# Optimization experiments

Measured on AMD Instinct MI355X. Metric: run time of the kernel, lower is better.

The kernel has to match this reference:

```python
import jax, jax.numpy as jnp
import numpy as np

N, E, G = 50000, 640000, 1024
D, RD, H = 128, 200, 512
NUM_ATOM_FEATS, ATOM_VOCAB = 9, 64
NUM_BOND_FEATS, BOND_VOCAB = 3, 16


def setup_inputs() -> dict:
    key = jax.random.key(0)
    ks = jax.random.split(key, 24)
    inp = {
        "x_feat": jax.random.randint(ks[0], (N, NUM_ATOM_FEATS), 0, ATOM_VOCAB),
        "edge_index": jax.random.randint(ks[1], (2, E), 0, N),
        "edge_attr_feat": jax.random.randint(ks[2], (E, NUM_BOND_FEATS), 0, BOND_VOCAB),
        "batch": jnp.sort(jax.random.randint(ks[3], (N,), 0, G)),
        "rdkit_feats": jax.random.normal(ks[4], (G, RD), dtype=jnp.float32),
        # learned params
        "atom_emb": jax.random.normal(ks[5], (NUM_ATOM_FEATS, ATOM_VOCAB, D), dtype=jnp.float32) * 0.02,
        "bond_emb": jax.random.normal(ks[6], (NUM_BOND_FEATS, BOND_VOCAB, D), dtype=jnp.float32) * 0.02,
        "conv1_w1": jax.random.normal(ks[7], (D, D), dtype=jnp.float32) / np.sqrt(D),
        "conv1_b1": jnp.zeros((D,), jnp.float32),
        "conv1_w2": jax.random.normal(ks[8], (D, D), dtype=jnp.float32) / np.sqrt(D),
        "conv1_b2": jnp.zeros((D,), jnp.float32),
        "conv2_w1": jax.random.normal(ks[9], (D, D), dtype=jnp.float32) / np.sqrt(D),
        "conv2_b1": jnp.zeros((D,), jnp.float32),
        "conv2_w2": jax.random.normal(ks[10], (D, D), dtype=jnp.float32) / np.sqrt(D),
        "conv2_b2": jnp.zeros((D,), jnp.float32),
        "mlp_w1": jax.random.normal(ks[11], (D + RD, H), dtype=jnp.float32) / np.sqrt(D + RD),
        "mlp_b1": jnp.zeros((H,), jnp.float32),
        "mlp_w2": jax.random.normal(ks[12], (H, H // 2), dtype=jnp.float32) / np.sqrt(H),
        "mlp_b2": jnp.zeros((H // 2,), jnp.float32),
        "mlp_w3": jax.random.normal(ks[13], (H // 2, 1), dtype=jnp.float32) / np.sqrt(H // 2),
        "mlp_b3": jnp.zeros((1,), jnp.float32),
    }
    return inp


def _gine_conv(x, edge_index, edge_attr, w1, b1, w2, b2, eps=0.0):
    # PyG GINEConv: out = nn((1+eps)*x + sum_{j in N(i)} relu(x_j + e_ji))
    src, dst = edge_index[0], edge_index[1]
    msg = jax.nn.relu(x[src] + edge_attr)               # [E, D]
    agg = jax.ops.segment_sum(msg, dst, num_segments=x.shape[0])  # [N, D]
    h = (1.0 + eps) * x + agg
    h = jax.nn.relu(h @ w1 + b1)
    return h @ w2 + b2


def reference(x_feat, edge_index, edge_attr_feat, batch, rdkit_feats,
              atom_emb, bond_emb,
              conv1_w1, conv1_b1, conv1_w2, conv1_b2,
              conv2_w1, conv2_b1, conv2_w2, conv2_b2,
              mlp_w1, mlp_b1, mlp_w2, mlp_b2, mlp_w3, mlp_b3):
    # AtomEncoder / BondEncoder: sum of per-feature categorical embeddings
    x = atom_emb[jnp.arange(NUM_ATOM_FEATS)[None, :], x_feat].sum(axis=1)          # [N, D]
    edge_attr = bond_emb[jnp.arange(NUM_BOND_FEATS)[None, :], edge_attr_feat].sum(axis=1)  # [E, D]

    x = _gine_conv(x, edge_index, edge_attr, conv1_w1, conv1_b1, conv1_w2, conv1_b2)
    x = _gine_conv(x, edge_index, edge_attr, conv2_w1, conv2_b1, conv2_w2, conv2_b2)

    # global mean pool over graphs
    sums = jax.ops.segment_sum(x, batch, num_segments=G)                # [G, D]
    counts = jax.ops.segment_sum(jnp.ones((x.shape[0],), x.dtype), batch, num_segments=G)
    pooled = sums / jnp.maximum(counts, 1.0)[:, None]

    h = jnp.concatenate([pooled, rdkit_feats], axis=1)                  # [G, D+RD]
    h = jax.nn.relu(h @ mlp_w1 + mlp_b1)   # dropout is identity in eval mode
    h = jax.nn.relu(h @ mlp_w2 + mlp_b2)
    return h @ mlp_w3 + mlp_b3                                          # [G, 1]
```

## Files before the change

### kernel.cpp

```cpp
#include <hip/hip_runtime.h>

#define N_NODES 50000
#define N_EDGES 640000
#define N_GRAPH 1024
#define D 128
#define RD 200
#define CAP 64

typedef __attribute__((ext_vector_type(4))) float f32x4;
typedef __attribute__((ext_vector_type(8))) float f32x8;
typedef __attribute__((ext_vector_type(4))) _Float16 half4;
typedef __attribute__((ext_vector_type(8))) _Float16 half8;

__global__ void k_prep(const float* __restrict__ w0, const float* __restrict__ w1,
                       const float* __restrict__ w2, const float* __restrict__ w3,
                       const float* __restrict__ mw1, const float* __restrict__ mw2,
                       const float* __restrict__ emb,
                       _Float16* __restrict__ cWf,
                       _Float16* __restrict__ W1f,
                       _Float16* __restrict__ W2f,
                       _Float16* __restrict__ embh,
                       int* __restrict__ deg) {
  int t = blockIdx.x * 256 + threadIdx.x;
  if (t < N_NODES) deg[t] = 0;
  if (t < 8192) {
    int mat = t >> 11, r = t & 2047;
    int frag = r >> 6, lane = r & 63;
    int n0 = frag >> 2, kk = frag & 3;
    int n = n0 * 16 + (lane & 15);
    int kb = (lane >> 4) * 8 + kk * 32;
    const float* W = (mat == 0) ? w0 : (mat == 1) ? w1 : (mat == 2) ? w2 : w3;
    half8 o;
#pragma unroll
    for (int j = 0; j < 8; ++j) o[j] = (_Float16)W[(kb + j) * D + n];
    *(half8*)&cWf[((size_t)mat * 2048 + r) * 8] = o;
  } else if (t < 8192 + 22528) {
    int u = t - 8192;
    int frag = u >> 6, lane = u & 63;
    int n0 = frag / 11, kk = frag % 11;
    int n = n0 * 16 + (lane & 15);
    int kb = (lane >> 4) * 8 + kk * 32;
    half8 o;
#pragma unroll
    for (int j = 0; j < 8; ++j) {
      int k = kb + j;
      o[j] = (k < 328) ? (_Float16)mw1[k * 512 + n] : (_Float16)0.f;
    }
    *(half8*)&W1f[(size_t)u * 8] = o;
  } else if (t < 8192 + 22528 + 16384) {
    int u = t - 8192 - 22528;
    int frag = u >> 6, lane = u & 63;
    int n0 = frag >> 4, kk = frag & 15;
    int n = n0 * 16 + (lane & 15);
    int kb = (lane >> 4) * 8 + kk * 32;
    half8 o;
#pragma unroll
    for (int j = 0; j < 8; ++j) o[j] = (_Float16)mw2[(kb + j) * 256 + n];
    *(half8*)&W2f[(size_t)u * 8] = o;
  } else if (t < 8192 + 22528 + 16384 + 9216) {
    int u = t - 8192 - 22528 - 16384;
    float4 v0 = *(const float4*)&emb[(size_t)u * 8];
    float4 v1 = *(const float4*)&emb[(size_t)u * 8 + 4];
    half8 o;
    o[0] = (_Float16)v0.x; o[1] = (_Float16)v0.y; o[2] = (_Float16)v0.z; o[3] = (_Float16)v0.w;
    o[4] = (_Float16)v1.x; o[5] = (_Float16)v1.y; o[6] = (_Float16)v1.z; o[7] = (_Float16)v1.w;
    *(half8*)&embh[(size_t)u * 8] = o;
  }
}

__global__ void k_atom_count(const int* __restrict__ xf, const _Float16* __restrict__ embh,
                             _Float16* __restrict__ x16,
                             const int* __restrict__ ei, const int* __restrict__ bondf,
                             const int* __restrict__ batch,
                             int* __restrict__ deg, int2* __restrict__ drep,
                             int* __restrict__ gstart) {
  if (blockIdx.x < 3125) {
    int t = blockIdx.x * 256 + threadIdx.x;
    int node = t >> 4, c = (t & 15) << 3;
    if ((t & 15) == 0) {
      int b = batch[node];
      int prev = (node == 0) ? -1 : batch[node - 1];
      for (int g = prev + 1; g <= b; ++g) gstart[g] = node;
      if (node == N_NODES - 1)
        for (int g = b + 1; g <= N_GRAPH; ++g) gstart[g] = N_NODES;
    }
    int v[9];
#pragma unroll
    for (int f = 0; f < 9; ++f) v[f] = xf[node * 9 + f];
    f32x8 a = (f32x8)(0.f);
#pragma unroll
    for (int f = 0; f < 9; ++f) {
      half8 e8 = *(const half8*)&embh[(size_t)(f * 64 + v[f]) * D + c];
      a += __builtin_convertvector(e8, f32x8);
    }
    half8 o;
#pragma unroll
    for (int tt = 0; tt < 8; ++tt) o[tt] = (_Float16)a[tt];
    *(half8*)&x16[(size_t)node * D + c] = o;
  } else {
    int e = (blockIdx.x - 3125) * 256 + threadIdx.x;
    if (e < N_EDGES) {
      int d = ei[N_EDGES + e];
      int rank = atomicAdd(&deg[d], 1);
      int s = ei[e];
      int f0 = bondf[e * 3], f1 = bondf[e * 3 + 1], f2 = bondf[e * 3 + 2];
      drep[e] = make_int2(d | (rank << 16), s | (f0 << 16) | (f1 << 20) | (f2 << 24));
    }
  }
}

__global__ void k_fill(const int2* __restrict__ drep, int* __restrict__ csr1) {
  int e = blockIdx.x * 256 + threadIdx.x;
  if (e >= N_EDGES) return;
  int2 v = drep[e];
  int d = v.x & 0xFFFF;
  int rank = ((unsigned)v.x) >> 16;
  if (rank < CAP) csr1[(d << 6) | rank] = v.y;
}

__global__ __launch_bounds__(256) void k_agg(
    const _Float16* __restrict__ X, const int* __restrict__ deg,
    const int* __restrict__ csr1, const float* __restrict__ bemb,
    _Float16* __restrict__ out) {
  __shared__ half8 sB[48 * 16];
  for (int t = threadIdx.x; t < 768; t += blockDim.x) {
    float4 v0 = *(const float4*)&bemb[t * 8];
    float4 v1 = *(const float4*)&bemb[t * 8 + 4];
    half8 h;
    h[0] = (_Float16)v0.x; h[1] = (_Float16)v0.y; h[2] = (_Float16)v0.z; h[3] = (_Float16)v0.w;
    h[4] = (_Float16)v1.x; h[5] = (_Float16)v1.y; h[6] = (_Float16)v1.z; h[7] = (_Float16)v1.w;
    sB[t] = h;
  }
  __syncthreads();
  int lane = threadIdx.x & 63;
  int quad = lane >> 4, l15 = lane & 15, c8 = l15 * 8;
  int wid = blockIdx.x * 4 + (threadIdx.x >> 6);
  int nw = gridDim.x * 4;
  if (wid >= N_NODES) return;
  int pdeg = deg[wid];
  int pcreg = csr1[(wid << 6) + lane];
  for (int i = wid; i < N_NODES; i += nw) {
    int degn = pdeg;
    int creg = pcreg;
    int i2 = (i + nw < N_NODES) ? i + nw : i;
    pdeg = deg[i2];
    pcreg = csr1[(i2 << 6) + lane];
    int dq = degn > CAP ? CAP : degn;
    f32x8 ac0 = (f32x8)(0.f), ac1 = (f32x8)(0.f);
    for (int jb = 0; jb < dq; jb += 8) {
      unsigned e0v = (unsigned)__shfl(creg, jb + quad);
      unsigned e1v = (unsigned)__shfl(creg, jb + 4 + quad);
      if (jb + quad < dq) {
        half8 x0 = *(const half8*)&X[(size_t)(e0v & 0xFFFF) * D + c8];
        unsigned p0 = e0v >> 16;
        half8 m0h = (x0 + sB[(p0 & 15) * 16 + l15]) +
                    (sB[256 + ((p0 >> 4) & 15) * 16 + l15] + sB[512 + (p0 >> 8) * 16 + l15]);
        f32x8 g0 = __builtin_convertvector(m0h, f32x8);
#pragma unroll
        for (int tt = 0; tt < 8; ++tt) ac0[tt] += fmaxf(g0[tt], 0.f);
      }
      if (jb + 4 + quad < dq) {
        half8 x1 = *(const half8*)&X[(size_t)(e1v & 0xFFFF) * D + c8];
        unsigned p1 = e1v >> 16;
        half8 m1h = (x1 + sB[(p1 & 15) * 16 + l15]) +
                    (sB[256 + ((p1 >> 4) & 15) * 16 + l15] + sB[512 + (p1 >> 8) * 16 + l15]);
        f32x8 g1 = __builtin_convertvector(m1h, f32x8);
#pragma unroll
        for (int tt = 0; tt < 8; ++tt) ac1[tt] += fmaxf(g1[tt], 0.f);
      }
    }
    f32x8 acc = ac0 + ac1;
#pragma unroll
    for (int tt = 0; tt < 8; ++tt) {
      acc[tt] += __shfl_xor(acc[tt], 16);
      acc[tt] += __shfl_xor(acc[tt], 32);
    }
    if (quad == 0) {
      half8 sr = *(const half8*)&X[(size_t)i * D + c8];
      f32x8 o = __builtin_convertvector(sr, f32x8) + acc;
      half8 oh;
#pragma unroll
      for (int tt = 0; tt < 8; ++tt) oh[tt] = (_Float16)o[tt];
      *(half8*)&out[(size_t)i * D + c8] = oh;
    }
  }
}

__global__ __launch_bounds__(256) void k_conv(
    const _Float16* __restrict__ A,
    const _Float16* __restrict__ W1f, const float* __restrict__ b1,
    const _Float16* __restrict__ W2f, const float* __restrict__ b2,
    _Float16* __restrict__ O16) {
  __shared__ _Float16 sW[2048 * 8];
  __shared__ _Float16 sI[128 * 136];
  int tid = threadIdx.x, w = tid >> 6, lane = tid & 63;
  int m0 = blockIdx.x * 128;
  int col16 = lane & 15, q = lane >> 4;
  for (int t = tid; t < 2048; t += 256)
    *(float4*)&sW[t * 8] = *(const float4*)&W1f[(size_t)t * 8];
  half8 afr[2][4];
#pragma unroll
  for (int f = 0; f < 2; ++f) {
    int row = m0 + w * 32 + f * 16 + col16;
    if (row >= N_NODES) row = N_NODES - 1;
    const _Float16* Ar = A + (size_t)row * D + q * 8;
#pragma unroll
    for (int kk = 0; kk < 4; ++kk) afr[f][kk] = *(const half8*)(Ar + kk * 32);
  }
  __syncthreads();
#pragma unroll
  for (int n0 = 0; n0 < 8; ++n0) {
    f32x4 a0 = {0.f, 0.f, 0.f, 0.f}, a1 = {0.f, 0.f, 0.f, 0.f};
#pragma unroll
    for (int kk = 0; kk < 4; ++kk) {
      half8 b = *(const half8*)&sW[((n0 * 4 + kk) * 64 + lane) * 8];
      a0 = __builtin_amdgcn_mfma_f32_16x16x32_f16(afr[0][kk], b, a0, 0, 0, 0);
      a1 = __builtin_amdgcn_mfma_f32_16x16x32_f16(afr[1][kk], b, a1, 0, 0, 0);
    }
    float bb = b1[n0 * 16 + col16];
#pragma unroll
    for (int r = 0; r < 4; ++r) {
      sI[(w * 32 + q * 4 + r) * 136 + n0 * 16 + col16] = (_Float16)fmaxf(a0[r] + bb, 0.f);
      sI[(w * 32 + 16 + q * 4 + r) * 136 + n0 * 16 + col16] = (_Float16)fmaxf(a1[r] + bb, 0.f);
    }
  }
  __syncthreads();
  for (int t = tid; t < 2048; t += 256)
    *(float4*)&sW[t * 8] = *(const float4*)&W2f[(size_t)t * 8];
  half8 a2[2][4];
#pragma unroll
  for (int f = 0; f < 2; ++f) {
    const _Float16* tr = &sI[(w * 32 + f * 16 + col16) * 136 + q * 8];
#pragma unroll
    for (int kk = 0; kk < 4; ++kk) a2[f][kk] = *(const half8*)(tr + kk * 32);
  }
  __syncthreads();
#pragma unroll
  for (int n0 = 0; n0 < 8; ++n0) {
    f32x4 a0 = {0.f, 0.f, 0.f, 0.f}, a1 = {0.f, 0.f, 0.f, 0.f};
#pragma unroll
    for (int kk = 0; kk < 4; ++kk) {
      half8 b = *(const half8*)&sW[((n0 * 4 + kk) * 64 + lane) * 8];
      a0 = __builtin_amdgcn_mfma_f32_16x16x32_f16(a2[0][kk], b, a0, 0, 0, 0);
      a1 = __builtin_amdgcn_mfma_f32_16x16x32_f16(a2[1][kk], b, a1, 0, 0, 0);
    }
    int col = n0 * 16 + col16;
    float bb = b2[col];
#pragma unroll
    for (int r = 0; r < 4; ++r) {
      int r0 = m0 + w * 32 + q * 4 + r;
      int r1 = r0 + 16;
      if (r0 < N_NODES) O16[(size_t)r0 * D + col] = (_Float16)(a0[r] + bb);
      if (r1 < N_NODES) O16[(size_t)r1 * D + col] = (_Float16)(a1[r] + bb);
    }
  }
}

__global__ __launch_bounds__(256) void k_pool(
    const _Float16* __restrict__ x, const int* __restrict__ gstart,
    const float* __restrict__ rdkit, _Float16* __restrict__ hcat,
    const float* __restrict__ B3, float* __restrict__ out) {
  int g = blockIdx.x * 4 + (threadIdx.x >> 6);
  if (g >= N_GRAPH) return;
  int lane = threadIdx.x & 63;
  int half_ = lane >> 5;
  int c4 = (lane & 31) * 4;
  int lo = gstart[g];
  int hi = gstart[g + 1];
  f32x4 a = {0.f, 0.f, 0.f, 0.f};
  for (int i = lo + half_; i < hi; i += 2) {
    half4 v = *(const half4*)&x[(size_t)i * D + c4];
    a += __builtin_convertvector(v, f32x4);
  }
#pragma unroll
  for (int t = 0; t < 4; ++t) a[t] += __shfl_xor(a[t], 32);
  float inv = 1.f / fmaxf((float)(hi - lo), 1.f);
  if (half_ == 0) {
    half4 o;
    o.x = (_Float16)(a[0] * inv); o.y = (_Float16)(a[1] * inv);
    o.z = (_Float16)(a[2] * inv); o.w = (_Float16)(a[3] * inv);
    *(half4*)&hcat[(size_t)g * 352 + c4] = o;
  }
  for (int r = lane; r < RD; r += 64)
    hcat[(size_t)g * 352 + D + r] = (_Float16)rdkit[(size_t)g * RD + r];
  if (lane < 24) hcat[(size_t)g * 352 + 328 + lane] = (_Float16)0.f;
  if (lane == 0) out[g] = B3[0];
}

__global__ __launch_bounds__(512) void k_mlp(
    const _Float16* __restrict__ A, const _Float16* __restrict__ W1f,
    const float* __restrict__ B1, const _Float16* __restrict__ W2f,
    const float* __restrict__ B2, const float* __restrict__ W3,
    float* __restrict__ out) {
  __shared__ _Float16 sH1[16 * 520];
  int tid = threadIdx.x, w = tid >> 6, lane = tid & 63;
  int mt = blockIdx.x;
  int col16 = lane & 15, q = lane >> 4;
  {
    half8 afr[11];
    const _Float16* Ar = A + (size_t)(mt * 16 + col16) * 352 + q * 8;
#pragma unroll
    for (int kk = 0; kk < 11; ++kk) afr[kk] = *(const half8*)(Ar + kk * 32);
#pragma unroll
    for (int ng = 0; ng < 4; ++ng) {
      int n0 = w * 4 + ng;
      f32x4 acc = {0.f, 0.f, 0.f, 0.f};
#pragma unroll
      for (int kk = 0; kk < 11; ++kk) {
        half8 b = *(const half8*)&W1f[(size_t)((n0 * 11 + kk) * 64 + lane) * 8];
        acc = __builtin_amdgcn_mfma_f32_16x16x32_f16(afr[kk], b, acc, 0, 0, 0);
      }
      int col = n0 * 16 + col16;
      float bb = B1[col];
#pragma unroll
      for (int r = 0; r < 4; ++r)
        sH1[(q * 4 + r) * 520 + col] = (_Float16)fmaxf(acc[r] + bb, 0.f);
    }
  }
  __syncthreads();
  {
    half8 a2[16];
    const _Float16* Ar = &sH1[col16 * 520 + q * 8];
#pragma unroll
    for (int kk = 0; kk < 16; ++kk) a2[kk] = *(const half8*)(Ar + kk * 32);
    float p[4] = {0.f, 0.f, 0.f, 0.f};
#pragma unroll
    for (int ng = 0; ng < 2; ++ng) {
      int n0 = w * 2 + ng;
      f32x4 acc = {0.f, 0.f, 0.f, 0.f};
#pragma unroll
      for (int kk = 0; kk < 16; ++kk) {
        half8 b = *(const half8*)&W2f[(size_t)((n0 * 16 + kk) * 64 + lane) * 8];
        acc = __builtin_amdgcn_mfma_f32_16x16x32_f16(a2[kk], b, acc, 0, 0, 0);
      }
      int col = n0 * 16 + col16;
      float bb = B2[col], w3 = W3[col];
#pragma unroll
      for (int r = 0; r < 4; ++r) p[r] += fmaxf(acc[r] + bb, 0.f) * w3;
    }
#pragma unroll
    for (int r = 0; r < 4; ++r) {
      p[r] += __shfl_xor(p[r], 1);
      p[r] += __shfl_xor(p[r], 2);
      p[r] += __shfl_xor(p[r], 4);
      p[r] += __shfl_xor(p[r], 8);
    }
    if (col16 == 0) {
#pragma unroll
      for (int r = 0; r < 4; ++r)
        atomicAdd(&out[mt * 16 + q * 4 + r], p[r]);
    }
  }
}

extern "C" void kernel_launch(void* const* d_in, const int* in_sizes, int n_in,
                              void* d_out, int out_size, void* d_ws, size_t ws_size,
                              hipStream_t stream) {
  const int* x_feat = (const int*)d_in[0];
  const int* ei = (const int*)d_in[1];
  const int* bondf = (const int*)d_in[2];
  const int* batch = (const int*)d_in[3];
  const float* rdkit = (const float*)d_in[4];
  const float* atom_emb = (const float*)d_in[5];
  const float* bond_emb = (const float*)d_in[6];
  const float* c1w1 = (const float*)d_in[7];
  const float* c1b1 = (const float*)d_in[8];
  const float* c1w2 = (const float*)d_in[9];
  const float* c1b2 = (const float*)d_in[10];
  const float* c2w1 = (const float*)d_in[11];
  const float* c2b1 = (const float*)d_in[12];
  const float* c2w2 = (const float*)d_in[13];
  const float* c2b2 = (const float*)d_in[14];
  const float* mw1 = (const float*)d_in[15];
  const float* mb1 = (const float*)d_in[16];
  const float* mw2 = (const float*)d_in[17];
  const float* mb2 = (const float*)d_in[18];
  const float* mw3 = (const float*)d_in[19];
  const float* mb3 = (const float*)d_in[20];
  float* out = (float*)d_out;

  char* ws = (char*)d_ws;
  size_t off = 0;
  auto alloc = [&](size_t bytes) {
    void* p = ws + off;
    off += (bytes + 255) & ~(size_t)255;
    return p;
  };
  _Float16* x16a = (_Float16*)alloc((size_t)N_NODES * D * 2);
  _Float16* x16b = (_Float16*)alloc((size_t)N_NODES * D * 2);
  _Float16* h16 = (_Float16*)alloc((size_t)N_NODES * D * 2);
  _Float16* x2_16 = (_Float16*)alloc((size_t)N_NODES * D * 2);
  int* deg = (int*)alloc((size_t)N_NODES * 4);
  int* csr1 = (int*)alloc((size_t)N_NODES * CAP * 4);
  int2* drep = (int2*)alloc((size_t)N_EDGES * 8);
  int* gstart = (int*)alloc((size_t)(N_GRAPH + 1) * 4);
  _Float16* hcat16 = (_Float16*)alloc((size_t)N_GRAPH * 352 * 2);
  _Float16* cWf = (_Float16*)alloc((size_t)4 * 2048 * 8 * 2);
  _Float16* W1f = (_Float16*)alloc((size_t)352 * 64 * 8 * 2);
  _Float16* W2f = (_Float16*)alloc((size_t)256 * 64 * 8 * 2);
  _Float16* embh = (_Float16*)alloc((size_t)9 * 64 * D * 2);

  k_prep<<<256, 256, 0, stream>>>(c1w1, c1w2, c2w1, c2w2, mw1, mw2, atom_emb,
                                  cWf, W1f, W2f, embh, deg);
  k_atom_count<<<3125 + 2500, 256, 0, stream>>>(x_feat, embh, x16a,
                                                ei, bondf, batch,
                                                deg, drep, gstart);
  k_fill<<<(N_EDGES + 255) / 256, 256, 0, stream>>>(drep, csr1);

  int ctiles = (N_NODES + 127) / 128;
  k_agg<<<2048, 256, 0, stream>>>(x16a, deg, csr1, bond_emb, h16);
  k_conv<<<ctiles, 256, 0, stream>>>(h16, cWf + 0 * 16384, c1b1,
                                     cWf + 1 * 16384, c1b2, x16b);
  k_agg<<<2048, 256, 0, stream>>>(x16b, deg, csr1, bond_emb, h16);
  k_conv<<<ctiles, 256, 0, stream>>>(h16, cWf + 2 * 16384, c2b1,
                                     cWf + 3 * 16384, c2b2, x2_16);

  k_pool<<<N_GRAPH / 4, 256, 0, stream>>>(x2_16, gstart, rdkit, hcat16, mb3, out);
  k_mlp<<<N_GRAPH / 16, 512, 0, stream>>>(hcat16, W1f, mb1, W2f, mb2, mw3, out);

  (void)in_sizes; (void)n_in; (void)out_size; (void)ws_size;
}
```

Measured before the change: 266.1 us.

## Fuse prep, atom encoding, and CSR fill; merge pooling into MLP head

Folds weight-fragment prep and degree zeroing into the atom-encoder kernel, which now reads the fp32 atom embeddings directly instead of a converted fp16 copy. The edge counting and CSR scatter become a single kernel, removing the intermediate drep buffer and one launch. The mean pool is merged into the MLP kernel through shared memory, eliminating the hcat round trip and another launch. In exchange, pooling runs on only 64 blocks, which lowers parallelism for that phase.

```diff
diff --git a/kernel.cpp b/kernel.cpp
--- a/kernel.cpp
+++ b/kernel.cpp
@@ -12,68 +12,16 @@
 typedef __attribute__((ext_vector_type(4))) _Float16 half4;
 typedef __attribute__((ext_vector_type(8))) _Float16 half8;
 
-__global__ void k_prep(const float* __restrict__ w0, const float* __restrict__ w1,
-                       const float* __restrict__ w2, const float* __restrict__ w3,
-                       const float* __restrict__ mw1, const float* __restrict__ mw2,
-                       const float* __restrict__ emb,
-                       _Float16* __restrict__ cWf,
-                       _Float16* __restrict__ W1f,
-                       _Float16* __restrict__ W2f,
-                       _Float16* __restrict__ embh,
-                       int* __restrict__ deg) {
-  int t = blockIdx.x * 256 + threadIdx.x;
-  if (t < N_NODES) deg[t] = 0;
-  if (t < 8192) {
-    int mat = t >> 11, r = t & 2047;
-    int frag = r >> 6, lane = r & 63;
-    int n0 = frag >> 2, kk = frag & 3;
-    int n = n0 * 16 + (lane & 15);
-    int kb = (lane >> 4) * 8 + kk * 32;
-    const float* W = (mat == 0) ? w0 : (mat == 1) ? w1 : (mat == 2) ? w2 : w3;
-    half8 o;
-#pragma unroll
-    for (int j = 0; j < 8; ++j) o[j] = (_Float16)W[(kb + j) * D + n];
-    *(half8*)&cWf[((size_t)mat * 2048 + r) * 8] = o;
-  } else if (t < 8192 + 22528) {
-    int u = t - 8192;
-    int frag = u >> 6, lane = u & 63;
-    int n0 = frag / 11, kk = frag % 11;
-    int n = n0 * 16 + (lane & 15);
-    int kb = (lane >> 4) * 8 + kk * 32;
-    half8 o;
-#pragma unroll
-    for (int j = 0; j < 8; ++j) {
-      int k = kb + j;
-      o[j] = (k < 328) ? (_Float16)mw1[k * 512 + n] : (_Float16)0.f;
-    }
-    *(half8*)&W1f[(size_t)u * 8] = o;
-  } else if (t < 8192 + 22528 + 16384) {
-    int u = t - 8192 - 22528;
-    int frag = u >> 6, lane = u & 63;
-    int n0 = frag >> 4, kk = frag & 15;
-    int n = n0 * 16 + (lane & 15);
-    int kb = (lane >> 4) * 8 + kk * 32;
-    half8 o;
-#pragma unroll
-    for (int j = 0; j < 8; ++j) o[j] = (_Float16)mw2[(kb + j) * 256 + n];
-    *(half8*)&W2f[(size_t)u * 8] = o;
-  } else if (t < 8192 + 22528 + 16384 + 9216) {
-    int u = t - 8192 - 22528 - 16384;
-    float4 v0 = *(const float4*)&emb[(size_t)u * 8];
-    float4 v1 = *(const float4*)&emb[(size_t)u * 8 + 4];
-    half8 o;
-    o[0] = (_Float16)v0.x; o[1] = (_Float16)v0.y; o[2] = (_Float16)v0.z; o[3] = (_Float16)v0.w;
-    o[4] = (_Float16)v1.x; o[5] = (_Float16)v1.y; o[6] = (_Float16)v1.z; o[7] = (_Float16)v1.w;
-    *(half8*)&embh[(size_t)u * 8] = o;
-  }
-}
-
-__global__ void k_atom_count(const int* __restrict__ xf, const _Float16* __restrict__ embh,
-                             _Float16* __restrict__ x16,
-                             const int* __restrict__ ei, const int* __restrict__ bondf,
-                             const int* __restrict__ batch,
-                             int* __restrict__ deg, int2* __restrict__ drep,
-                             int* __restrict__ gstart) {
+__global__ void k_pre(const float* __restrict__ emb,
+                      const int* __restrict__ xf, const int* __restrict__ batch,
+                      const float* __restrict__ w0, const float* __restrict__ w1,
+                      const float* __restrict__ w2, const float* __restrict__ w3,
+                      const float* __restrict__ mw1, const float* __restrict__ mw2,
+                      _Float16* __restrict__ cWf,
+                      _Float16* __restrict__ W1f,
+                      _Float16* __restrict__ W2f,
+                      _Float16* __restrict__ x16, int* __restrict__ deg,
+                      int* __restrict__ gstart) {
   if (blockIdx.x < 3125) {
     int t = blockIdx.x * 256 + threadIdx.x;
     int node = t >> 4, c = (t & 15) << 3;
@@ -90,32 +38,67 @@
     f32x8 a = (f32x8)(0.f);
 #pragma unroll
     for (int f = 0; f < 9; ++f) {
-      half8 e8 = *(const half8*)&embh[(size_t)(f * 64 + v[f]) * D + c];
-      a += __builtin_convertvector(e8, f32x8);
+      const float* er = &emb[(size_t)(f * 64 + v[f]) * D + c];
+      float4 v0 = *(const float4*)er;
+      float4 v1 = *(const float4*)(er + 4);
+      a[0] += v0.x; a[1] += v0.y; a[2] += v0.z; a[3] += v0.w;
+      a[4] += v1.x; a[5] += v1.y; a[6] += v1.z; a[7] += v1.w;
     }
     half8 o;
 #pragma unroll
     for (int tt = 0; tt < 8; ++tt) o[tt] = (_Float16)a[tt];
     *(half8*)&x16[(size_t)node * D + c] = o;
   } else {
-    int e = (blockIdx.x - 3125) * 256 + threadIdx.x;
-    if (e < N_EDGES) {
-      int d = ei[N_EDGES + e];
-      int rank = atomicAdd(&deg[d], 1);
-      int s = ei[e];
-      int f0 = bondf[e * 3], f1 = bondf[e * 3 + 1], f2 = bondf[e * 3 + 2];
-      drep[e] = make_int2(d | (rank << 16), s | (f0 << 16) | (f1 << 20) | (f2 << 24));
-    }
-  }
-}
-
-__global__ void k_fill(const int2* __restrict__ drep, int* __restrict__ csr1) {
+    int u = (blockIdx.x - 3125) * 256 + threadIdx.x;
+    if (u < N_NODES) deg[u] = 0;
+    if (u < 8192) {
+      int mat = u >> 11, r = u & 2047;
+      int frag = r >> 6, lane = r & 63;
+      int n0 = frag >> 2, kk = frag & 3;
+      int n = n0 * 16 + (lane & 15);
+      int kb = (lane >> 4) * 8 + kk * 32;
+      const float* W = (mat == 0) ? w0 : (mat == 1) ? w1 : (mat == 2) ? w2 : w3;
+      half8 o;
+#pragma unroll
+      for (int j = 0; j < 8; ++j) o[j] = (_Float16)W[(kb + j) * D + n];
+      *(half8*)&cWf[((size_t)mat * 2048 + r) * 8] = o;
+    } else if (u < 8192 + 22528) {
+      int t2 = u - 8192;
+      int frag = t2 >> 6, lane = t2 & 63;
+      int n0 = frag / 11, kk = frag % 11;
+      int n = n0 * 16 + (lane & 15);
+      int kb = (lane >> 4) * 8 + kk * 32;
+      half8 o;
+#pragma unroll
+      for (int j = 0; j < 8; ++j) {
+        int k = kb + j;
+        o[j] = (k < 328) ? (_Float16)mw1[k * 512 + n] : (_Float16)0.f;
+      }
+      *(half8*)&W1f[(size_t)t2 * 8] = o;
+    } else if (u < 8192 + 22528 + 16384) {
+      int t2 = u - 8192 - 22528;
+      int frag = t2 >> 6, lane = t2 & 63;
+      int n0 = frag >> 4, kk = frag & 15;
+      int n = n0 * 16 + (lane & 15);
+      int kb = (lane >> 4) * 8 + kk * 32;
+      half8 o;
+#pragma unroll
+      for (int j = 0; j < 8; ++j) o[j] = (_Float16)mw2[(kb + j) * 256 + n];
+      *(half8*)&W2f[(size_t)t2 * 8] = o;
+    }
+  }
+}
+
+__global__ void k_fill(const int* __restrict__ ei, const int* __restrict__ bondf,
+                       int* __restrict__ deg, int* __restrict__ csr1) {
   int e = blockIdx.x * 256 + threadIdx.x;
   if (e >= N_EDGES) return;
-  int2 v = drep[e];
-  int d = v.x & 0xFFFF;
-  int rank = ((unsigned)v.x) >> 16;
-  if (rank < CAP) csr1[(d << 6) | rank] = v.y;
+  int d = ei[N_EDGES + e];
+  int rank = atomicAdd(&deg[d], 1);
+  int s = ei[e];
+  int f0 = bondf[e * 3], f1 = bondf[e * 3 + 1], f2 = bondf[e * 3 + 2];
+  if (rank < CAP)
+    csr1[(d << 6) | rank] = s | (f0 << 16) | (f1 << 20) | (f2 << 24);
 }
 
 __global__ __launch_bounds__(256) void k_agg(
@@ -256,49 +239,53 @@
   }
 }
 
-__global__ __launch_bounds__(256) void k_pool(
+__global__ __launch_bounds__(512) void k_head(
     const _Float16* __restrict__ x, const int* __restrict__ gstart,
-    const float* __restrict__ rdkit, _Float16* __restrict__ hcat,
-    const float* __restrict__ B3, float* __restrict__ out) {
-  int g = blockIdx.x * 4 + (threadIdx.x >> 6);
-  if (g >= N_GRAPH) return;
-  int lane = threadIdx.x & 63;
-  int half_ = lane >> 5;
-  int c4 = (lane & 31) * 4;
-  int lo = gstart[g];
-  int hi = gstart[g + 1];
-  f32x4 a = {0.f, 0.f, 0.f, 0.f};
-  for (int i = lo + half_; i < hi; i += 2) {
-    half4 v = *(const half4*)&x[(size_t)i * D + c4];
-    a += __builtin_convertvector(v, f32x4);
-  }
-#pragma unroll
-  for (int t = 0; t < 4; ++t) a[t] += __shfl_xor(a[t], 32);
-  float inv = 1.f / fmaxf((float)(hi - lo), 1.f);
-  if (half_ == 0) {
-    half4 o;
-    o.x = (_Float16)(a[0] * inv); o.y = (_Float16)(a[1] * inv);
-    o.z = (_Float16)(a[2] * inv); o.w = (_Float16)(a[3] * inv);
-    *(half4*)&hcat[(size_t)g * 352 + c4] = o;
-  }
-  for (int r = lane; r < RD; r += 64)
-    hcat[(size_t)g * 352 + D + r] = (_Float16)rdkit[(size_t)g * RD + r];
-  if (lane < 24) hcat[(size_t)g * 352 + 328 + lane] = (_Float16)0.f;
-  if (lane == 0) out[g] = B3[0];
-}
-
-__global__ __launch_bounds__(512) void k_mlp(
-    const _Float16* __restrict__ A, const _Float16* __restrict__ W1f,
-    const float* __restrict__ B1, const _Float16* __restrict__ W2f,
-    const float* __restrict__ B2, const float* __restrict__ W3,
+    const float* __restrict__ rdkit,
+    const _Float16* __restrict__ W1f, const float* __restrict__ B1,
+    const _Float16* __restrict__ W2f, const float* __restrict__ B2,
+    const float* __restrict__ W3, const float* __restrict__ B3,
     float* __restrict__ out) {
+  __shared__ _Float16 sH[16 * 360];
   __shared__ _Float16 sH1[16 * 520];
   int tid = threadIdx.x, w = tid >> 6, lane = tid & 63;
   int mt = blockIdx.x;
   int col16 = lane & 15, q = lane >> 4;
+
+  {
+    int half_ = lane >> 5;
+    int c4 = (lane & 31) * 4;
+#pragma unroll
+    for (int gg = 0; gg < 2; ++gg) {
+      int row = w * 2 + gg;
+      int g = mt * 16 + row;
+      int lo = gstart[g];
+      int hi = gstart[g + 1];
+      f32x4 a = {0.f, 0.f, 0.f, 0.f};
+      for (int i = lo + half_; i < hi; i += 2) {
+        half4 v = *(const half4*)&x[(size_t)i * D + c4];
+        a += __builtin_convertvector(v, f32x4);
+      }
+#pragma unroll
+      for (int t = 0; t < 4; ++t) a[t] += __shfl_xor(a[t], 32);
+      float inv = 1.f / fmaxf((float)(hi - lo), 1.f);
+      if (half_ == 0) {
+        half4 o;
+        o.x = (_Float16)(a[0] * inv); o.y = (_Float16)(a[1] * inv);
+        o.z = (_Float16)(a[2] * inv); o.w = (_Float16)(a[3] * inv);
+        *(half4*)&sH[row * 360 + c4] = o;
+      }
+      for (int r = lane; r < RD; r += 64)
+        sH[row * 360 + D + r] = (_Float16)rdkit[(size_t)g * RD + r];
+      if (lane < 24) sH[row * 360 + 328 + lane] = (_Float16)0.f;
+      if (lane == 0) out[g] = B3[0];
+    }
+  }
+  __syncthreads();
+
   {
     half8 afr[11];
-    const _Float16* Ar = A + (size_t)(mt * 16 + col16) * 352 + q * 8;
+    const _Float16* Ar = &sH[col16 * 360 + q * 8];
 #pragma unroll
     for (int kk = 0; kk < 11; ++kk) afr[kk] = *(const half8*)(Ar + kk * 32);
 #pragma unroll
@@ -318,6 +305,7 @@
     }
   }
   __syncthreads();
+
   {
     half8 a2[16];
     const _Float16* Ar = &sH1[col16 * 520 + q * 8];
@@ -392,20 +380,15 @@
   _Float16* x2_16 = (_Float16*)alloc((size_t)N_NODES * D * 2);
   int* deg = (int*)alloc((size_t)N_NODES * 4);
   int* csr1 = (int*)alloc((size_t)N_NODES * CAP * 4);
-  int2* drep = (int2*)alloc((size_t)N_EDGES * 8);
   int* gstart = (int*)alloc((size_t)(N_GRAPH + 1) * 4);
-  _Float16* hcat16 = (_Float16*)alloc((size_t)N_GRAPH * 352 * 2);
   _Float16* cWf = (_Float16*)alloc((size_t)4 * 2048 * 8 * 2);
   _Float16* W1f = (_Float16*)alloc((size_t)352 * 64 * 8 * 2);
   _Float16* W2f = (_Float16*)alloc((size_t)256 * 64 * 8 * 2);
-  _Float16* embh = (_Float16*)alloc((size_t)9 * 64 * D * 2);
-
-  k_prep<<<256, 256, 0, stream>>>(c1w1, c1w2, c2w1, c2w2, mw1, mw2, atom_emb,
-                                  cWf, W1f, W2f, embh, deg);
-  k_atom_count<<<3125 + 2500, 256, 0, stream>>>(x_feat, embh, x16a,
-                                                ei, bondf, batch,
-                                                deg, drep, gstart);
-  k_fill<<<(N_EDGES + 255) / 256, 256, 0, stream>>>(drep, csr1);
+
+  k_pre<<<3125 + 196, 256, 0, stream>>>(atom_emb, x_feat, batch,
+                                        c1w1, c1w2, c2w1, c2w2, mw1, mw2,
+                                        cWf, W1f, W2f, x16a, deg, gstart);
+  k_fill<<<(N_EDGES + 255) / 256, 256, 0, stream>>>(ei, bondf, deg, csr1);
 
   int ctiles = (N_NODES + 127) / 128;
   k_agg<<<2048, 256, 0, stream>>>(x16a, deg, csr1, bond_emb, h16);
@@ -415,8 +398,8 @@
   k_conv<<<ctiles, 256, 0, stream>>>(h16, cWf + 2 * 16384, c2b1,
                                      cWf + 3 * 16384, c2b2, x2_16);
 
-  k_pool<<<N_GRAPH / 4, 256, 0, stream>>>(x2_16, gstart, rdkit, hcat16, mb3, out);
-  k_mlp<<<N_GRAPH / 16, 512, 0, stream>>>(hcat16, W1f, mb1, W2f, mb2, mw3, out);
+  k_head<<<N_GRAPH / 16, 512, 0, stream>>>(x2_16, gstart, rdkit,
+                                           W1f, mb1, W2f, mb2, mw3, mb3, out);
 
   (void)in_sizes; (void)n_in; (void)out_size; (void)ws_size;
 }
```

Measured after the change: 275.6 us. 3.6% more time.
